# Kernel optimization log

Measured on AMD Instinct MI355X. Metric: run time of the kernel, lower is better.

Reference implementation:

```python
import jax, jax.numpy as jnp
import numpy as np

N = 400_000
G = 160
C_IN, C_OUT = 64, 38
K = 27  # 3x3x3 kernel offsets


def _build_neighbor_map(rng):
    # sample N unique occupied voxel coordinates, sorted by ravelled key
    keys = np.sort(rng.choice(G ** 3, size=N, replace=False))
    coords = np.stack(np.unravel_index(keys, (G, G, G)), axis=1).astype(np.int64)  # [N,3]
    nbr = np.full((K, N), N, dtype=np.int32)  # N = padding index -> zero feature row
    k = 0
    for dx in (-1, 0, 1):
        for dy in (-1, 0, 1):
            for dz in (-1, 0, 1):
                nc = coords + np.array([dx, dy, dz])
                valid = np.all((nc >= 0) & (nc < G), axis=1)
                nkey = (nc[:, 0] * G + nc[:, 1]) * G + nc[:, 2]
                pos = np.searchsorted(keys, nkey)
                pos_c = np.clip(pos, 0, N - 1)
                found = valid & (keys[pos_c] == nkey)
                nbr[k] = np.where(found, pos_c, N).astype(np.int32)
                k += 1
    return nbr


def setup_inputs() -> dict:
    key = jax.random.key(0)
    k1, k2, k3 = jax.random.split(key, 3)
    rng = np.random.default_rng(0)
    neighbor_idx = jnp.asarray(_build_neighbor_map(rng))
    features = jax.random.normal(k1, (N, C_IN), dtype=jnp.float32)
    # kaiming_normal fan_out (relu): std = sqrt(2 / fan_out), fan_out = K * C_out
    std1 = (2.0 / (K * C_OUT)) ** 0.5
    std2 = (2.0 / (K * C_OUT)) ** 0.5
    W1 = jax.random.normal(k2, (K, C_IN, C_OUT), dtype=jnp.float32) * std1
    W2 = jax.random.normal(k3, (K, C_OUT, C_OUT), dtype=jnp.float32) * std2
    return {"features": features, "neighbor_idx": neighbor_idx, "W1": W1, "W2": W2}


def _sparse_conv(feat, W, neighbor_idx):
    # gather-GEMM-scatter: out[i] = sum_k W[k]^T feat[nbr[k,i]]
    fp = jnp.concatenate([feat, jnp.zeros((1, feat.shape[1]), feat.dtype)], axis=0)
    out = jnp.zeros((feat.shape[0], W.shape[2]), feat.dtype)
    for k in range(K):  # fixed structural loop over 27 kernel offsets
        out = out + fp[neighbor_idx[k]] @ W[k]
    return out


def reference(features, neighbor_idx, W1, W2):
    h = _sparse_conv(features, W1, neighbor_idx)
    h = jax.nn.gelu(h, approximate=False)  # torch nn.GELU default = exact
    return _sparse_conv(h, W2, neighbor_idx)
```

## Files before the change

kernel.cpp:

```cpp
#include <hip/hip_runtime.h>
#include <math.h>

#define NPTS 400000
#define K27  27
#define WSTRIDE 4096

typedef unsigned short u16;
typedef __bf16 bf16x8 __attribute__((ext_vector_type(8)));
typedef float  f32x4  __attribute__((ext_vector_type(4)));
typedef __attribute__((address_space(1))) void gvoid;
typedef __attribute__((address_space(3))) void lvoid;

__device__ __forceinline__ u16 f2bf(float f) {
    unsigned u = __float_as_uint(f);
    u += 0x7FFFu + ((u >> 16) & 1u);
    return (u16)(u >> 16);
}
__device__ __forceinline__ unsigned pack2(float lo, float hi) {
    return (unsigned)f2bf(lo) | ((unsigned)f2bf(hi) << 16);
}
__device__ __forceinline__ bf16x8 pack8(float4 x, float4 y) {
    union { uint4 u; bf16x8 v; } r;
    r.u.x = pack2(x.x, x.y); r.u.y = pack2(x.z, x.w);
    r.u.z = pack2(y.x, y.y); r.u.w = pack2(y.z, y.w);
    return r.v;
}
__device__ __forceinline__ bf16x8 zero8() {
    union { uint4 u; bf16x8 v; } r;
    r.u.x = 0; r.u.y = 0; r.u.z = 0; r.u.w = 0;
    return r.v;
}

__global__ void prep_w(const float* __restrict__ W1, const float* __restrict__ W2,
                       u16* __restrict__ W1t, u16* __restrict__ W2t,
                       u16* __restrict__ hpad, u16* __restrict__ fpad)
{
    int i = blockIdx.x * 256 + threadIdx.x;
    if (i < 64) {
        hpad[i] = 0;
        if (fpad) fpad[i] = 0;
    }
    const int TOT = K27 * 48 * 64;
    if (i >= TOT) return;
    int k  = i / (48 * 64);
    int r  = i % (48 * 64);
    int n  = r >> 6;
    int kc = r & 63;
    u16 w1 = 0, w2 = 0;
    if (n < 38) {
        w1 = f2bf(W1[(k * 64 + kc) * 38 + n]);
        if (kc < 38) w2 = f2bf(W2[(k * 38 + kc) * 38 + n]);
    }
    int os = r ^ ((n & 7) << 3);
    W1t[k * WSTRIDE + os] = w1;
    W2t[k * WSTRIDE + os] = w2;
}

__global__ void prep_feat(const float* __restrict__ F, u16* __restrict__ Fb)
{
    size_t i = (size_t)blockIdx.x * 256 + threadIdx.x;
    const size_t TOT = (size_t)NPTS * 64 / 8;
    if (i >= TOT) return;
    const float4* fp = (const float4*)(F + i * 8);
    float4 a = fp[0], b = fp[1];
    uint4 v;
    v.x = pack2(a.x, a.y); v.y = pack2(a.z, a.w);
    v.z = pack2(b.x, b.y); v.w = pack2(b.z, b.w);
    *(uint4*)(Fb + i * 8) = v;
}

template<int LAYER, bool BF16IN>
__global__ __launch_bounds__(256, 4)
void spconv(const void* __restrict__ in_, const int* __restrict__ nbr,
            const u16* __restrict__ Wt, void* __restrict__ out_)
{
    __shared__ __align__(16) u16 wbuf[2][WSTRIDE];

    const int t    = threadIdx.x;
    const int wave = t >> 6;
    const int lane = t & 63;
    const int quad = lane >> 4;
    const int l16  = lane & 15;

    int bid;
    {
        const int nwg = NPTS / 128, q = nwg / 8, r = nwg % 8;
        int x = blockIdx.x % 8, o = blockIdx.x / 8;
        bid = (x < r ? x * (q + 1) : r * (q + 1) + (x - r) * q) + o;
    }
    const int rbase = bid * 128 + wave * 32;
    const int swz   = (l16 & 7) << 3;

    f32x4 acc[2][3] = {};
    bf16x8 aP[2][2], aQ[2][2];
    int iP[2], iQ[2];

    #define GATHER_BF16(dst, ids)                                             \
        {                                                                     \
            const u16* F = (const u16*)in_;                                   \
            _Pragma("unroll")                                                 \
            for (int rt = 0; rt < 2; ++rt) {                                  \
                const u16* rowp = F + (size_t)(ids)[rt] * 64 + quad * 8;      \
                (dst)[rt][0] = *(const bf16x8*)(rowp);                        \
                (dst)[rt][1] = *(const bf16x8*)(rowp + 32);                   \
            }                                                                 \
        }
    #define GATHER_F32(dst, ids)                                              \
        {                                                                     \
            const float* F = (const float*)in_;                               \
            _Pragma("unroll")                                                 \
            for (int rt = 0; rt < 2; ++rt) {                                  \
                if ((ids)[rt] < NPTS) {                                       \
                    const float* rowp = F + (size_t)(ids)[rt] * 64 + quad * 8;\
                    float4 f0 = *(const float4*)(rowp);                       \
                    float4 f1 = *(const float4*)(rowp + 4);                   \
                    float4 f2 = *(const float4*)(rowp + 32);                  \
                    float4 f3 = *(const float4*)(rowp + 36);                  \
                    (dst)[rt][0] = pack8(f0, f1);                             \
                    (dst)[rt][1] = pack8(f2, f3);                             \
                } else {                                                      \
                    (dst)[rt][0] = zero8();                                   \
                    (dst)[rt][1] = zero8();                                   \
                }                                                             \
            }                                                                 \
        }
    #define GATHER(dst, ids) { if (BF16IN) GATHER_BF16(dst, ids) else GATHER_F32(dst, ids) }

    #define STAGE_W(KW, BSEL)                                                 \
        {                                                                     \
            const u16* g_ = Wt + (size_t)(KW) * WSTRIDE + t * 8;              \
            u16* l_ = &wbuf[(BSEL)][t * 8];                                   \
            __builtin_amdgcn_global_load_lds((gvoid*)(g_),                    \
                                             (lvoid*)(l_), 16, 0, 0);         \
            __builtin_amdgcn_global_load_lds((gvoid*)(g_ + 2048),             \
                                             (lvoid*)(l_ + 2048), 16, 0, 0);  \
        }

    #pragma unroll
    for (int rt = 0; rt < 2; ++rt) iP[rt] = nbr[rbase + rt * 16 + l16];
    GATHER(aP, iP);
    #pragma unroll
    for (int rt = 0; rt < 2; ++rt) iQ[rt] = nbr[(size_t)NPTS + rbase + rt * 16 + l16];
    STAGE_W(0, 0);
    STAGE_W(1, 1);
    __builtin_amdgcn_sched_barrier(0);
    asm volatile("s_waitcnt vmcnt(2)");
    __builtin_amdgcn_s_barrier();
    __builtin_amdgcn_sched_barrier(0);

    #define ITER(KK, ACUR, ANXT, ICUR, INXT)                                  \
      {                                                                       \
        const int k_ = (KK);                                                  \
                         \
        bf16x8 bfr[3][2];                                                     \
        {                                                                     \
            const u16* wb = &wbuf[k_ & 1][0];                                 \
            _Pragma("unroll")                                                 \
            for (int nt = 0; nt < 3; ++nt)                                    \
                _Pragma("unroll")                                             \
                for (int ks = 0; ks < 2; ++ks)                                \
                    bfr[nt][ks] = *(const bf16x8*)&wb[(nt * 16 + l16) * 64    \
                                        + ((ks * 32 + quad * 8) ^ swz)];      \
        }                                                                     \
        {                                                                     \
            int kf = k_ + 2; if (kf > K27 - 1) kf = K27 - 1;                  \
            const int* nr = nbr + (size_t)kf * NPTS + rbase;                  \
            _Pragma("unroll")                                                 \
            for (int rt = 0; rt < 2; ++rt) INXT[rt] = nr[rt * 16 + l16];      \
        }                                                                     \
        GATHER(ANXT, ICUR);                                                   \
        __builtin_amdgcn_sched_barrier(0);                                    \
                                    \
        _Pragma("unroll")                                                     \
        for (int ks = 0; ks < 2; ++ks)                                        \
            _Pragma("unroll")                                                 \
            for (int rt = 0; rt < 2; ++rt)                                    \
                _Pragma("unroll")                                             \
                for (int nt = 0; nt < 3; ++nt)                                \
                    acc[rt][nt] = __builtin_amdgcn_mfma_f32_16x16x32_bf16(    \
                        ACUR[rt][ks], bfr[nt][ks], acc[rt][nt], 0, 0, 0);     \
        __builtin_amdgcn_sched_barrier(0);                                    \
                         \
        if (BF16IN) { asm volatile("s_waitcnt vmcnt(6)"); }                   \
        else        { asm volatile("s_waitcnt vmcnt(10)"); }                  \
        __builtin_amdgcn_s_barrier();                                         \
        __builtin_amdgcn_sched_barrier(0);                                    \
                         \
        {                                                                     \
            int kw = k_ + 2; if (kw > K27 - 1) kw = K27 - 1;                  \
            STAGE_W(kw, k_ & 1);                                              \
        }                                                                     \
        __builtin_amdgcn_sched_barrier(0);                                    \
      }

    for (int k = 0; k < K27 - 1; k += 2) {
        ITER(k,     aP, aQ, iQ, iP);
        ITER(k + 1, aQ, aP, iP, iQ);
    }
    ITER(K27 - 1, aP, aQ, iQ, iP);

    if (LAYER == 1) {
        u16* h = (u16*)out_;
        #pragma unroll
        for (int rt = 0; rt < 2; ++rt) {
            #pragma unroll
            for (int r = 0; r < 4; ++r) {
                size_t ro = (size_t)(rbase + rt * 16 + quad * 4 + r) * 64;
                #pragma unroll
                for (int nt = 0; nt < 3; ++nt) {
                    float x = acc[rt][nt][r];
                    float g = 0.5f * x * (1.0f + erff(x * 0.70710678118654752f));
                    h[ro + nt * 16 + l16] = f2bf(g);
                }
                h[ro + 48 + l16] = 0;
            }
        }
    } else {
        float* out = (float*)out_;
        #pragma unroll
        for (int rt = 0; rt < 2; ++rt) {
            #pragma unroll
            for (int nt = 0; nt < 3; ++nt) {
                int col = nt * 16 + l16;
                if (col < 38) {
                    #pragma unroll
                    for (int r = 0; r < 4; ++r) {
                        int row = rbase + rt * 16 + quad * 4 + r;
                        out[(size_t)row * 38 + col] = acc[rt][nt][r];
                    }
                }
            }
        }
    }
    #undef ITER
    #undef STAGE_W
    #undef GATHER
    #undef GATHER_BF16
    #undef GATHER_F32
}

extern "C" void kernel_launch(void* const* d_in, const int* in_sizes, int n_in,
                              void* d_out, int out_size, void* d_ws, size_t ws_size,
                              hipStream_t stream)
{
    const float* feat = (const float*)d_in[0];
    const int*   nbr  = (const int*)  d_in[1];
    const float* W1   = (const float*)d_in[2];
    const float* W2   = (const float*)d_in[3];

    const size_t hbytes = (size_t)(NPTS + 1) * 64 * 2;
    const size_t wbytes = (size_t)K27 * WSTRIDE * 2;

    char* ws  = (char*)d_ws;
    u16* h    = (u16*)ws;
    u16* W1t  = (u16*)(ws + hbytes);
    u16* W2t  = (u16*)(ws + hbytes + wbytes);
    u16* Fb   = (u16*)(ws + hbytes + 2 * wbytes);
    const bool full = ws_size >= hbytes * 2 + 2 * wbytes;

    prep_w<<<(K27 * 48 * 64 + 255) / 256, 256, 0, stream>>>(
        W1, W2, W1t, W2t,
        h + (size_t)NPTS * 64,
        full ? Fb + (size_t)NPTS * 64 : (u16*)nullptr);

    const int nblk = NPTS / 128;
    if (full) {
        prep_feat<<<(int)(((size_t)NPTS * 64 / 8 + 255) / 256), 256, 0, stream>>>(feat, Fb);
        spconv<1, true ><<<nblk, 256, 0, stream>>>(Fb,   nbr, W1t, h);
    } else {
        spconv<1, false><<<nblk, 256, 0, stream>>>(feat, nbr, W1t, h);
    }
    spconv<2, true ><<<nblk, 256, 0, stream>>>(h, nbr, W2t, d_out);
}
```

Baseline: 412.0 us.

## Deepen neighbor-gather pipeline to three stages and raise MFMA wave priority

Adds a third register buffer for gathered feature rows and neighbor indices, so the gather for offset k+2 is issued while MFMAs for offset k run; the main loop now unrolls by three with a prologue that preloads two offsets. MFMA blocks are wrapped in s_setprio to favour the issuing wave, and launch bounds drop from 4 to 3 waves per SIMD to leave room for the extra registers. The aim is to hide more gather latency. The vmcnt waits are unchanged and may still force earlier gathers to complete, and the lower occupancy costs latency hiding across waves.

```diff
diff --git a/kernel.cpp b/kernel.cpp
--- a/kernel.cpp
+++ b/kernel.cpp
@@ -70,7 +70,7 @@
 }
 
 template<int LAYER, bool BF16IN>
-__global__ __launch_bounds__(256, 4)
+__global__ __launch_bounds__(256, 3)
 void spconv(const void* __restrict__ in_, const int* __restrict__ nbr,
             const u16* __restrict__ Wt, void* __restrict__ out_)
 {
@@ -92,8 +92,8 @@
     const int swz   = (l16 & 7) << 3;
 
     f32x4 acc[2][3] = {};
-    bf16x8 aP[2][2], aQ[2][2];
-    int iP[2], iQ[2];
+    bf16x8 aP[2][2], aQ[2][2], aR[2][2];
+    int jP[2], jQ[2], jR[2];
 
     #define GATHER_BF16(dst, ids)                                             \
         {                                                                     \
@@ -136,11 +136,17 @@
                                              (lvoid*)(l_ + 2048), 16, 0, 0);  \
         }
 
-    #pragma unroll
-    for (int rt = 0; rt < 2; ++rt) iP[rt] = nbr[rbase + rt * 16 + l16];
-    GATHER(aP, iP);
-    #pragma unroll
-    for (int rt = 0; rt < 2; ++rt) iQ[rt] = nbr[(size_t)NPTS + rbase + rt * 16 + l16];
+    {
+        int i0[2], i1[2];
+        #pragma unroll
+        for (int rt = 0; rt < 2; ++rt) i0[rt] = nbr[rbase + rt * 16 + l16];
+        GATHER(aP, i0);
+        #pragma unroll
+        for (int rt = 0; rt < 2; ++rt) i1[rt] = nbr[(size_t)NPTS + rbase + rt * 16 + l16];
+        GATHER(aQ, i1);
+        #pragma unroll
+        for (int rt = 0; rt < 2; ++rt) jP[rt] = nbr[(size_t)2 * NPTS + rbase + rt * 16 + l16];
+    }
     STAGE_W(0, 0);
     STAGE_W(1, 1);
     __builtin_amdgcn_sched_barrier(0);
@@ -148,10 +154,9 @@
     __builtin_amdgcn_s_barrier();
     __builtin_amdgcn_sched_barrier(0);
 
-    #define ITER(KK, ACUR, ANXT, ICUR, INXT)                                  \
+    #define ITER(KK, ACUR, AISS, JUSE, JLOAD)                                 \
       {                                                                       \
         const int k_ = (KK);                                                  \
-                         \
         bf16x8 bfr[3][2];                                                     \
         {                                                                     \
             const u16* wb = &wbuf[k_ & 1][0];                                 \
@@ -163,14 +168,14 @@
                                         + ((ks * 32 + quad * 8) ^ swz)];      \
         }                                                                     \
         {                                                                     \
-            int kf = k_ + 2; if (kf > K27 - 1) kf = K27 - 1;                  \
+            int kf = k_ + 3; if (kf > K27 - 1) kf = K27 - 1;                  \
             const int* nr = nbr + (size_t)kf * NPTS + rbase;                  \
             _Pragma("unroll")                                                 \
-            for (int rt = 0; rt < 2; ++rt) INXT[rt] = nr[rt * 16 + l16];      \
+            for (int rt = 0; rt < 2; ++rt) JLOAD[rt] = nr[rt * 16 + l16];     \
         }                                                                     \
-        GATHER(ANXT, ICUR);                                                   \
-        __builtin_amdgcn_sched_barrier(0);                                    \
-                                    \
+        GATHER(AISS, JUSE);                                                   \
+        __builtin_amdgcn_sched_barrier(0);                                    \
+        __builtin_amdgcn_s_setprio(1);                                        \
         _Pragma("unroll")                                                     \
         for (int ks = 0; ks < 2; ++ks)                                        \
             _Pragma("unroll")                                                 \
@@ -179,13 +184,12 @@
                 for (int nt = 0; nt < 3; ++nt)                                \
                     acc[rt][nt] = __builtin_amdgcn_mfma_f32_16x16x32_bf16(    \
                         ACUR[rt][ks], bfr[nt][ks], acc[rt][nt], 0, 0, 0);     \
-        __builtin_amdgcn_sched_barrier(0);                                    \
-                         \
+        __builtin_amdgcn_s_setprio(0);                                        \
+        __builtin_amdgcn_sched_barrier(0);                                    \
         if (BF16IN) { asm volatile("s_waitcnt vmcnt(6)"); }                   \
         else        { asm volatile("s_waitcnt vmcnt(10)"); }                  \
         __builtin_amdgcn_s_barrier();                                         \
         __builtin_amdgcn_sched_barrier(0);                                    \
-                         \
         {                                                                     \
             int kw = k_ + 2; if (kw > K27 - 1) kw = K27 - 1;                  \
             STAGE_W(kw, k_ & 1);                                              \
@@ -193,11 +197,11 @@
         __builtin_amdgcn_sched_barrier(0);                                    \
       }
 
-    for (int k = 0; k < K27 - 1; k += 2) {
-        ITER(k,     aP, aQ, iQ, iP);
-        ITER(k + 1, aQ, aP, iP, iQ);
-    }
-    ITER(K27 - 1, aP, aQ, iQ, iP);
+    for (int k = 0; k < K27; k += 3) {
+        ITER(k,     aP, aR, jP, jQ);
+        ITER(k + 1, aQ, aP, jQ, jR);
+        ITER(k + 2, aR, aQ, jR, jP);
+    }
 
     if (LAYER == 1) {
         u16* h = (u16*)out_;
```

New measurement: 415.1 us. Within noise of the previous version (+0.8%).

## Drop LDS weight staging; load weights per-wave from global/L2 with single-wave blocks

Applied to the files above, without the earlier changes.

Weights are no longer double-buffered in LDS through global_load_lds with block barriers. Each single-wave workgroup now reads its weight fragments straight from global memory, relying on L1/L2 caching, in a compact unswizzled layout. The block size shrinks from 256 to 64 threads, which removes barrier stalls. MFMA sections are also wrapped in s_setprio. The trade-off is more redundant global/L1 weight traffic per wave, plus weight loads in the critical path that could lengthen latency.

```diff
diff --git a/kernel.cpp b/kernel.cpp
--- a/kernel.cpp
+++ b/kernel.cpp
@@ -3,13 +3,11 @@
 
 #define NPTS 400000
 #define K27  27
-#define WSTRIDE 4096
+#define WTILE 3072
 
 typedef unsigned short u16;
 typedef __bf16 bf16x8 __attribute__((ext_vector_type(8)));
 typedef float  f32x4  __attribute__((ext_vector_type(4)));
-typedef __attribute__((address_space(1))) void gvoid;
-typedef __attribute__((address_space(3))) void lvoid;
 
 __device__ __forceinline__ u16 f2bf(float f) {
     unsigned u = __float_as_uint(f);
@@ -51,9 +49,8 @@
         w1 = f2bf(W1[(k * 64 + kc) * 38 + n]);
         if (kc < 38) w2 = f2bf(W2[(k * 38 + kc) * 38 + n]);
     }
-    int os = r ^ ((n & 7) << 3);
-    W1t[k * WSTRIDE + os] = w1;
-    W2t[k * WSTRIDE + os] = w2;
+    W1t[k * WTILE + r] = w1;
+    W2t[k * WTILE + r] = w2;
 }
 
 __global__ void prep_feat(const float* __restrict__ F, u16* __restrict__ Fb)
@@ -70,26 +67,22 @@
 }
 
 template<int LAYER, bool BF16IN>
-__global__ __launch_bounds__(256, 4)
+__global__ __launch_bounds__(64, 4)
 void spconv(const void* __restrict__ in_, const int* __restrict__ nbr,
             const u16* __restrict__ Wt, void* __restrict__ out_)
 {
-    __shared__ __align__(16) u16 wbuf[2][WSTRIDE];
-
-    const int t    = threadIdx.x;
-    const int wave = t >> 6;
-    const int lane = t & 63;
+    const int lane = threadIdx.x & 63;
     const int quad = lane >> 4;
     const int l16  = lane & 15;
 
     int bid;
     {
-        const int nwg = NPTS / 128, q = nwg / 8, r = nwg % 8;
+        const int nwg = NPTS / 32, q = nwg / 8, r = nwg % 8;
         int x = blockIdx.x % 8, o = blockIdx.x / 8;
         bid = (x < r ? x * (q + 1) : r * (q + 1) + (x - r) * q) + o;
     }
-    const int rbase = bid * 128 + wave * 32;
-    const int swz   = (l16 & 7) << 3;
+    const int rbase = bid * 32;
+    const u16* wlane = Wt + l16 * 64 + quad * 8;
 
     f32x4 acc[2][3] = {};
     bf16x8 aP[2][2], aQ[2][2];
@@ -126,41 +119,23 @@
         }
     #define GATHER(dst, ids) { if (BF16IN) GATHER_BF16(dst, ids) else GATHER_F32(dst, ids) }
 
-    #define STAGE_W(KW, BSEL)                                                 \
-        {                                                                     \
-            const u16* g_ = Wt + (size_t)(KW) * WSTRIDE + t * 8;              \
-            u16* l_ = &wbuf[(BSEL)][t * 8];                                   \
-            __builtin_amdgcn_global_load_lds((gvoid*)(g_),                    \
-                                             (lvoid*)(l_), 16, 0, 0);         \
-            __builtin_amdgcn_global_load_lds((gvoid*)(g_ + 2048),             \
-                                             (lvoid*)(l_ + 2048), 16, 0, 0);  \
-        }
-
     #pragma unroll
     for (int rt = 0; rt < 2; ++rt) iP[rt] = nbr[rbase + rt * 16 + l16];
     GATHER(aP, iP);
     #pragma unroll
     for (int rt = 0; rt < 2; ++rt) iQ[rt] = nbr[(size_t)NPTS + rbase + rt * 16 + l16];
-    STAGE_W(0, 0);
-    STAGE_W(1, 1);
-    __builtin_amdgcn_sched_barrier(0);
-    asm volatile("s_waitcnt vmcnt(2)");
-    __builtin_amdgcn_s_barrier();
-    __builtin_amdgcn_sched_barrier(0);
 
     #define ITER(KK, ACUR, ANXT, ICUR, INXT)                                  \
       {                                                                       \
         const int k_ = (KK);                                                  \
-                         \
         bf16x8 bfr[3][2];                                                     \
         {                                                                     \
-            const u16* wb = &wbuf[k_ & 1][0];                                 \
+            const u16* wk = wlane + (size_t)k_ * WTILE;                       \
             _Pragma("unroll")                                                 \
             for (int nt = 0; nt < 3; ++nt)                                    \
                 _Pragma("unroll")                                             \
                 for (int ks = 0; ks < 2; ++ks)                                \
-                    bfr[nt][ks] = *(const bf16x8*)&wb[(nt * 16 + l16) * 64    \
-                                        + ((ks * 32 + quad * 8) ^ swz)];      \
+                    bfr[nt][ks] = *(const bf16x8*)(wk + nt * 1024 + ks * 32); \
         }                                                                     \
         {                                                                     \
             int kf = k_ + 2; if (kf > K27 - 1) kf = K27 - 1;                  \
@@ -170,7 +145,7 @@
         }                                                                     \
         GATHER(ANXT, ICUR);                                                   \
         __builtin_amdgcn_sched_barrier(0);                                    \
-                                    \
+        __builtin_amdgcn_s_setprio(1);                                        \
         _Pragma("unroll")                                                     \
         for (int ks = 0; ks < 2; ++ks)                                        \
             _Pragma("unroll")                                                 \
@@ -179,17 +154,7 @@
                 for (int nt = 0; nt < 3; ++nt)                                \
                     acc[rt][nt] = __builtin_amdgcn_mfma_f32_16x16x32_bf16(    \
                         ACUR[rt][ks], bfr[nt][ks], acc[rt][nt], 0, 0, 0);     \
-        __builtin_amdgcn_sched_barrier(0);                                    \
-                         \
-        if (BF16IN) { asm volatile("s_waitcnt vmcnt(6)"); }                   \
-        else        { asm volatile("s_waitcnt vmcnt(10)"); }                  \
-        __builtin_amdgcn_s_barrier();                                         \
-        __builtin_amdgcn_sched_barrier(0);                                    \
-                         \
-        {                                                                     \
-            int kw = k_ + 2; if (kw > K27 - 1) kw = K27 - 1;                  \
-            STAGE_W(kw, k_ & 1);                                              \
-        }                                                                     \
+        __builtin_amdgcn_s_setprio(0);                                        \
         __builtin_amdgcn_sched_barrier(0);                                    \
       }
 
@@ -233,7 +198,6 @@
         }
     }
     #undef ITER
-    #undef STAGE_W
     #undef GATHER
     #undef GATHER_BF16
     #undef GATHER_F32
@@ -249,7 +213,7 @@
     const float* W2   = (const float*)d_in[3];
 
     const size_t hbytes = (size_t)(NPTS + 1) * 64 * 2;
-    const size_t wbytes = (size_t)K27 * WSTRIDE * 2;
+    const size_t wbytes = (size_t)K27 * WTILE * 2;
 
     char* ws  = (char*)d_ws;
     u16* h    = (u16*)ws;
@@ -263,12 +227,12 @@
         h + (size_t)NPTS * 64,
         full ? Fb + (size_t)NPTS * 64 : (u16*)nullptr);
 
-    const int nblk = NPTS / 128;
+    const int nblk = NPTS / 32;
     if (full) {
         prep_feat<<<(int)(((size_t)NPTS * 64 / 8 + 255) / 256), 256, 0, stream>>>(feat, Fb);
-        spconv<1, true ><<<nblk, 256, 0, stream>>>(Fb,   nbr, W1t, h);
+        spconv<1, true ><<<nblk, 64, 0, stream>>>(Fb,   nbr, W1t, h);
     } else {
-        spconv<1, false><<<nblk, 256, 0, stream>>>(feat, nbr, W1t, h);
-    }
-    spconv<2, true ><<<nblk, 256, 0, stream>>>(h, nbr, W2t, d_out);
-}
+        spconv<1, false><<<nblk, 64, 0, stream>>>(feat, nbr, W1t, h);
+    }
+    spconv<2, true ><<<nblk, 64, 0, stream>>>(h, nbr, W2t, d_out);
+}
```

After: 766.5 us. +86.0%, slower.

## Process kernel offsets in pairs per pipeline stage with deeper gather prefetch

Applied to the files above, without the earlier changes.

Restructures the 27-offset loop into super-iterations that each handle two offsets. Per stage it stages two weight tiles into LDS and keeps two offsets' gathers in flight, which halves the number of workgroup barriers and raises memory-level parallelism for the irregular neighbor gathers. It also switches to 32-bit byte-offset addressing and raises MFMA issue priority with s_setprio. In exchange register and LDS use roughly double (launch bounds drop from 4 to 3 waves per SIMD), which lowers occupancy, and the hand-tuned vmcnt counts must stay exactly matched to the new load counts.

```diff
diff --git a/kernel.cpp b/kernel.cpp
--- a/kernel.cpp
+++ b/kernel.cpp
@@ -70,11 +70,11 @@
 }
 
 template<int LAYER, bool BF16IN>
-__global__ __launch_bounds__(256, 4)
+__global__ __launch_bounds__(256, 3)
 void spconv(const void* __restrict__ in_, const int* __restrict__ nbr,
             const u16* __restrict__ Wt, void* __restrict__ out_)
 {
-    __shared__ __align__(16) u16 wbuf[2][WSTRIDE];
+    __shared__ __align__(16) u16 wbuf[2][2][WSTRIDE];
 
     const int t    = threadIdx.x;
     const int wave = t >> 6;
@@ -92,112 +92,138 @@
     const int swz   = (l16 & 7) << 3;
 
     f32x4 acc[2][3] = {};
-    bf16x8 aP[2][2], aQ[2][2];
-    int iP[2], iQ[2];
+    bf16x8 aP[2][2][2], aQ[2][2][2];
+    int iP[2][2], iQ[2][2];
 
     #define GATHER_BF16(dst, ids)                                             \
         {                                                                     \
-            const u16* F = (const u16*)in_;                                   \
+            const char* F8 = (const char*)in_;                                \
+            _Pragma("unroll")                                                 \
+            for (int ks = 0; ks < 2; ++ks)                                    \
             _Pragma("unroll")                                                 \
             for (int rt = 0; rt < 2; ++rt) {                                  \
-                const u16* rowp = F + (size_t)(ids)[rt] * 64 + quad * 8;      \
-                (dst)[rt][0] = *(const bf16x8*)(rowp);                        \
-                (dst)[rt][1] = *(const bf16x8*)(rowp + 32);                   \
+                unsigned off = (unsigned)(ids)[ks][rt] * 128u                 \
+                             + (unsigned)(quad * 16);                         \
+                (dst)[ks][rt][0] = *(const bf16x8*)(F8 + off);                \
+                (dst)[ks][rt][1] = *(const bf16x8*)(F8 + off + 64);           \
             }                                                                 \
         }
     #define GATHER_F32(dst, ids)                                              \
         {                                                                     \
-            const float* F = (const float*)in_;                               \
+            const char* F8 = (const char*)in_;                                \
+            _Pragma("unroll")                                                 \
+            for (int ks = 0; ks < 2; ++ks)                                    \
             _Pragma("unroll")                                                 \
             for (int rt = 0; rt < 2; ++rt) {                                  \
-                if ((ids)[rt] < NPTS) {                                       \
-                    const float* rowp = F + (size_t)(ids)[rt] * 64 + quad * 8;\
-                    float4 f0 = *(const float4*)(rowp);                       \
-                    float4 f1 = *(const float4*)(rowp + 4);                   \
-                    float4 f2 = *(const float4*)(rowp + 32);                  \
-                    float4 f3 = *(const float4*)(rowp + 36);                  \
-                    (dst)[rt][0] = pack8(f0, f1);                             \
-                    (dst)[rt][1] = pack8(f2, f3);                             \
+                if ((ids)[ks][rt] < NPTS) {                                   \
+                    unsigned off = (unsigned)(ids)[ks][rt] * 256u             \
+                                 + (unsigned)(quad * 32);                     \
+                    float4 f0 = *(const float4*)(F8 + off);                   \
+                    float4 f1 = *(const float4*)(F8 + off + 16);              \
+                    float4 f2 = *(const float4*)(F8 + off + 128);             \
+                    float4 f3 = *(const float4*)(F8 + off + 144);             \
+                    (dst)[ks][rt][0] = pack8(f0, f1);                         \
+                    (dst)[ks][rt][1] = pack8(f2, f3);                         \
                 } else {                                                      \
-                    (dst)[rt][0] = zero8();                                   \
-                    (dst)[rt][1] = zero8();                                   \
+                    (dst)[ks][rt][0] = zero8();                               \
+                    (dst)[ks][rt][1] = zero8();                               \
                 }                                                             \
             }                                                                 \
         }
     #define GATHER(dst, ids) { if (BF16IN) GATHER_BF16(dst, ids) else GATHER_F32(dst, ids) }
 
-    #define STAGE_W(KW, BSEL)                                                 \
-        {                                                                     \
-            const u16* g_ = Wt + (size_t)(KW) * WSTRIDE + t * 8;              \
-            u16* l_ = &wbuf[(BSEL)][t * 8];                                   \
-            __builtin_amdgcn_global_load_lds((gvoid*)(g_),                    \
-                                             (lvoid*)(l_), 16, 0, 0);         \
-            __builtin_amdgcn_global_load_lds((gvoid*)(g_ + 2048),             \
-                                             (lvoid*)(l_ + 2048), 16, 0, 0);  \
-        }
-
-    #pragma unroll
-    for (int rt = 0; rt < 2; ++rt) iP[rt] = nbr[rbase + rt * 16 + l16];
+    #define STAGE_WPAIR(KW, BSEL)                                             \
+        {                                                                     \
+            int kk0 = (KW);     if (kk0 > K27 - 1) kk0 = K27 - 1;             \
+            int kk1 = (KW) + 1; if (kk1 > K27 - 1) kk1 = K27 - 1;             \
+            const u16* g0 = Wt + (size_t)kk0 * WSTRIDE + t * 8;               \
+            const u16* g1 = Wt + (size_t)kk1 * WSTRIDE + t * 8;               \
+            u16* l0 = &wbuf[(BSEL)][0][t * 8];                                \
+            u16* l1 = &wbuf[(BSEL)][1][t * 8];                                \
+            __builtin_amdgcn_global_load_lds((gvoid*)g0, (lvoid*)l0, 16,0,0); \
+            __builtin_amdgcn_global_load_lds((gvoid*)(g0 + 2048),             \
+                                             (lvoid*)(l0 + 2048), 16,0,0);    \
+            __builtin_amdgcn_global_load_lds((gvoid*)g1, (lvoid*)l1, 16,0,0); \
+            __builtin_amdgcn_global_load_lds((gvoid*)(g1 + 2048),             \
+                                             (lvoid*)(l1 + 2048), 16,0,0);    \
+        }
+
+    #define MFMA_K(APAIR, KS2, BSEL, TILE)                                    \
+        {                                                                     \
+            bf16x8 bfr[3][2];                                                 \
+            const u16* wb = &wbuf[(BSEL)][(TILE)][0];                         \
+            _Pragma("unroll")                                                 \
+            for (int nt = 0; nt < 3; ++nt)                                    \
+                _Pragma("unroll")                                             \
+                for (int kq = 0; kq < 2; ++kq)                                \
+                    bfr[nt][kq] = *(const bf16x8*)&wb[(nt * 16 + l16) * 64    \
+                                        + ((kq * 32 + quad * 8) ^ swz)];      \
+            __builtin_amdgcn_s_setprio(1);                                    \
+            _Pragma("unroll")                                                 \
+            for (int kq = 0; kq < 2; ++kq)                                    \
+                _Pragma("unroll")                                             \
+                for (int rt = 0; rt < 2; ++rt)                                \
+                    _Pragma("unroll")                                         \
+                    for (int nt = 0; nt < 3; ++nt)                            \
+                        acc[rt][nt] = __builtin_amdgcn_mfma_f32_16x16x32_bf16(\
+                            (APAIR)[KS2][rt][kq], bfr[nt][kq],                \
+                            acc[rt][nt], 0, 0, 0);                           \
+            __builtin_amdgcn_s_setprio(0);                                    \
+        }
+
+    #define LOAD_IDX(dst, KF)                                                 \
+        {                                                                     \
+            int kf0 = (KF);     if (kf0 > K27 - 1) kf0 = K27 - 1;             \
+            int kf1 = (KF) + 1; if (kf1 > K27 - 1) kf1 = K27 - 1;             \
+            const int kfs[2] = {kf0, kf1};                                    \
+            _Pragma("unroll")                                                 \
+            for (int ks = 0; ks < 2; ++ks)                                    \
+            _Pragma("unroll")                                                 \
+            for (int rt = 0; rt < 2; ++rt) {                                  \
+                unsigned io = (unsigned)(kfs[ks] * NPTS + rbase + rt * 16     \
+                                         + l16) * 4u;                         \
+                (dst)[ks][rt] = *(const int*)((const char*)nbr + io);         \
+            }                                                                 \
+        }
+
+    LOAD_IDX(iP, 0);
     GATHER(aP, iP);
-    #pragma unroll
-    for (int rt = 0; rt < 2; ++rt) iQ[rt] = nbr[(size_t)NPTS + rbase + rt * 16 + l16];
-    STAGE_W(0, 0);
-    STAGE_W(1, 1);
+    LOAD_IDX(iQ, 2);
+    STAGE_WPAIR(0, 0);
+    STAGE_WPAIR(2, 1);
     __builtin_amdgcn_sched_barrier(0);
-    asm volatile("s_waitcnt vmcnt(2)");
+    asm volatile("s_waitcnt vmcnt(0)" ::: "memory");
     __builtin_amdgcn_s_barrier();
     __builtin_amdgcn_sched_barrier(0);
 
-    #define ITER(KK, ACUR, ANXT, ICUR, INXT)                                  \
+    #define SUPER(TT, ACUR, AISS, IUSE, ILOAD, BSEL)                          \
       {                                                                       \
-        const int k_ = (KK);                                                  \
-                         \
-        bf16x8 bfr[3][2];                                                     \
-        {                                                                     \
-            const u16* wb = &wbuf[k_ & 1][0];                                 \
-            _Pragma("unroll")                                                 \
-            for (int nt = 0; nt < 3; ++nt)                                    \
-                _Pragma("unroll")                                             \
-                for (int ks = 0; ks < 2; ++ks)                                \
-                    bfr[nt][ks] = *(const bf16x8*)&wb[(nt * 16 + l16) * 64    \
-                                        + ((ks * 32 + quad * 8) ^ swz)];      \
-        }                                                                     \
-        {                                                                     \
-            int kf = k_ + 2; if (kf > K27 - 1) kf = K27 - 1;                  \
-            const int* nr = nbr + (size_t)kf * NPTS + rbase;                  \
-            _Pragma("unroll")                                                 \
-            for (int rt = 0; rt < 2; ++rt) INXT[rt] = nr[rt * 16 + l16];      \
-        }                                                                     \
-        GATHER(ANXT, ICUR);                                                   \
+        const int t_ = (TT);                                                  \
+                              \
+        LOAD_IDX(ILOAD, 2 * t_ + 4);                                          \
+        GATHER(AISS, IUSE);                                                   \
         __builtin_amdgcn_sched_barrier(0);                                    \
-                                    \
-        _Pragma("unroll")                                                     \
-        for (int ks = 0; ks < 2; ++ks)                                        \
-            _Pragma("unroll")                                                 \
-            for (int rt = 0; rt < 2; ++rt)                                    \
-                _Pragma("unroll")                                             \
-                for (int nt = 0; nt < 3; ++nt)                                \
-                    acc[rt][nt] = __builtin_amdgcn_mfma_f32_16x16x32_bf16(    \
-                        ACUR[rt][ks], bfr[nt][ks], acc[rt][nt], 0, 0, 0);     \
+                                            \
+        MFMA_K(ACUR, 0, BSEL, 0);                                             \
+        MFMA_K(ACUR, 1, BSEL, 1);                                             \
         __builtin_amdgcn_sched_barrier(0);                                    \
-                         \
-        if (BF16IN) { asm volatile("s_waitcnt vmcnt(6)"); }                   \
-        else        { asm volatile("s_waitcnt vmcnt(10)"); }                  \
+                \
+        if (BF16IN) { asm volatile("s_waitcnt vmcnt(12)" ::: "memory"); }     \
+        else        { asm volatile("s_waitcnt vmcnt(20)" ::: "memory"); }     \
         __builtin_amdgcn_s_barrier();                                         \
         __builtin_amdgcn_sched_barrier(0);                                    \
-                         \
-        {                                                                     \
-            int kw = k_ + 2; if (kw > K27 - 1) kw = K27 - 1;                  \
-            STAGE_W(kw, k_ & 1);                                              \
-        }                                                                     \
+              \
+        STAGE_WPAIR(2 * t_ + 4, BSEL);                                        \
         __builtin_amdgcn_sched_barrier(0);                                    \
       }
 
-    for (int k = 0; k < K27 - 1; k += 2) {
-        ITER(k,     aP, aQ, iQ, iP);
-        ITER(k + 1, aQ, aP, iP, iQ);
-    }
-    ITER(K27 - 1, aP, aQ, iQ, iP);
+    for (int tt = 0; tt < 12; tt += 2) {
+        SUPER(tt,     aP, aQ, iQ, iP, 0);
+        SUPER(tt + 1, aQ, aP, iP, iQ, 1);
+    }
+    SUPER(12, aP, aQ, iQ, iP, 0);
+
+    MFMA_K(aQ, 0, 1, 0);
 
     if (LAYER == 1) {
         u16* h = (u16*)out_;
@@ -232,8 +258,10 @@
             }
         }
     }
-    #undef ITER
-    #undef STAGE_W
+    #undef SUPER
+    #undef LOAD_IDX
+    #undef MFMA_K
+    #undef STAGE_WPAIR
     #undef GATHER
     #undef GATHER_BF16
     #undef GATHER_F32
```

New measurement: 408.1 us. About the same (-0.9%).
